# Performance work log

Measured on AMD Instinct MI355X. Metric: run time of the kernel, lower is better.

## Reference

```python
import jax, jax.numpy as jnp
import numpy as np

DIM = 2048
N_HEADS = 32
N_KV_HEADS = 8
HEAD_DIM = DIM // N_HEADS  # 64
N_REP = N_HEADS // N_KV_HEADS
ROPE_BASE = 10000.0


def rope_tables(seq_len, dim):
    inv_freq = 1.0 / (ROPE_BASE ** (jnp.arange(0, dim, 2, dtype=jnp.float32) / dim))
    t = jnp.arange(seq_len, dtype=jnp.float32)
    freqs = jnp.outer(t, inv_freq)            # [S, dim/2]
    emb = jnp.concatenate([freqs, freqs], -1)  # [S, dim]
    return jnp.cos(emb), jnp.sin(emb)          # each [S, dim]


def rotate_half(x):
    x1, x2 = jnp.split(x, 2, axis=-1)
    return jnp.concatenate([-x2, x1], axis=-1)


def setup_inputs() -> dict:
    key = jax.random.key(0)
    k_x, k_q, k_k, k_v, k_o = jax.random.split(key, 5)
    B, S = 2, 2048
    scale = 0.02
    x = jax.random.normal(k_x, (B, S, DIM), dtype=jnp.float32)
    # torch Linear weights are [out, in]
    w_q = jax.random.normal(k_q, (N_HEADS * HEAD_DIM, DIM), dtype=jnp.float32) * scale
    w_k = jax.random.normal(k_k, (N_KV_HEADS * HEAD_DIM, DIM), dtype=jnp.float32) * scale
    w_v = jax.random.normal(k_v, (N_KV_HEADS * HEAD_DIM, DIM), dtype=jnp.float32) * scale
    w_o = jax.random.normal(k_o, (DIM, N_HEADS * HEAD_DIM), dtype=jnp.float32) * scale
    return {"x": x, "w_q": w_q, "w_k": w_k, "w_v": w_v, "w_o": w_o}


def reference(x, w_q, w_k, w_v, w_o):
    B, S, _ = x.shape
    # projections (torch Linear: x @ W^T), reshape to [B, H, S, D]
    q = jnp.einsum('bsd,ed->bse', x, w_q).reshape(B, S, N_HEADS, HEAD_DIM).transpose(0, 2, 1, 3)
    k = jnp.einsum('bsd,ed->bse', x, w_k).reshape(B, S, N_KV_HEADS, HEAD_DIM).transpose(0, 2, 1, 3)
    v = jnp.einsum('bsd,ed->bse', x, w_v).reshape(B, S, N_KV_HEADS, HEAD_DIM).transpose(0, 2, 1, 3)
    # RoPE
    cos, sin = rope_tables(S, HEAD_DIM)  # [S, D]
    cos = cos[None, None]
    sin = sin[None, None]
    q = q * cos + rotate_half(q) * sin
    k = k * cos + rotate_half(k) * sin
    # GQA: expand kv heads (repeat_interleave along head dim)
    k = jnp.repeat(k, N_REP, axis=1)
    v = jnp.repeat(v, N_REP, axis=1)
    # attention
    scores = jnp.einsum('bhqd,bhkd->bhqk', q, k) / jnp.sqrt(jnp.float32(HEAD_DIM))
    attn = jax.nn.softmax(scores, axis=-1)
    out = jnp.einsum('bhqk,bhkd->bhqd', attn, v)
    out = out.transpose(0, 2, 1, 3).reshape(B, S, N_HEADS * HEAD_DIM)
    return jnp.einsum('bse,de->bsd', out, w_o)
```

## Files before the change

kernel.cpp:

```cpp
#include <hip/hip_runtime.h>
#include <hip/hip_bf16.h>

typedef __attribute__((ext_vector_type(8))) short bf16x8;
typedef __attribute__((ext_vector_type(4))) short bf16x4s;
typedef __attribute__((ext_vector_type(4))) float f32x4;
typedef __attribute__((ext_vector_type(2))) unsigned int u32x2;
typedef unsigned int u32;

#define DIM 2048
#define NH 32
#define NKV 8
#define HD 64
#define BB 2
#define SS 2048
#define MROWS (BB*SS)
#define NQKV 3072
#define KDIM 2048
#define L2E 1.44269504f

__device__ __forceinline__ short f2bf(float f){
  u32 u = __float_as_uint(f);
  u32 r = u + 0x7fffu + ((u >> 16) & 1u);
  return (short)(r >> 16);
}
__device__ __forceinline__ float bf2f(short s){
  return __uint_as_float(((u32)(unsigned short)s) << 16);
}

__device__ __forceinline__ void gload16(const void* g, void* l){
  __builtin_amdgcn_global_load_lds((const __attribute__((address_space(1))) u32*)g,
                                   (__attribute__((address_space(3))) u32*)l, 16, 0, 0);
}

__global__ __launch_bounds__(256) void cvt_all_kernel(const float* __restrict__ x,
                                                      const float* __restrict__ wq,
                                                      const float* __restrict__ wk,
                                                      const float* __restrict__ wv,
                                                      const float* __restrict__ wo,
                                                      short* __restrict__ xb,
                                                      short* __restrict__ wqkvb,
                                                      short* __restrict__ wob,
                                                      float* __restrict__ cosT,
                                                      float* __restrict__ sinT){
  int bid = blockIdx.x;
  if (bid >= 18432){
    int idx = (bid-18432)*256 + threadIdx.x;
    int s = idx >> 5, i = idx & 31;
    float inv = powf(10000.f, -(float)i * (1.f/32.f));
    float f = (float)s * inv;
    cosT[idx] = cosf(f);
    sinT[idx] = sinf(f);
    return;
  }
  int i = bid*256 + threadIdx.x;
  const float* src; short* dst; int off;
  if      (bid <  8192){ src = x;  dst = xb;              off = 0; }
  else if (bid < 12288){ src = wq; dst = wqkvb;           off = 2097152; }
  else if (bid < 13312){ src = wk; dst = wqkvb+2048*2048; off = 3145728; }
  else if (bid < 14336){ src = wv; dst = wqkvb+2560*2048; off = 3407872; }
  else                 { src = wo; dst = wob;             off = 3670016; }
  int j = i - off;
  f32x4 v = ((const f32x4*)src)[j];
  bf16x4s o;
  #pragma unroll
  for (int t=0;t<4;++t) o[t] = f2bf(v[t]);
  ((bf16x4s*)dst)[j] = o;
}

__global__ __launch_bounds__(256) void vT_kernel(const short* __restrict__ qkv,
                                                 short* __restrict__ Vtg){
  __shared__ short T[64*72];
  const int tid = threadIdx.x;
  const int s0 = blockIdx.x*64, hkv = blockIdx.y, b = blockIdx.z;
  const short* vbase = qkv + (size_t)b*SS*NQKV + DIM + NKV*HD + hkv*HD;
  #pragma unroll
  for (int cc=0; cc<2; ++cc){
    int c = tid + cc*256;
    int s = c >> 3, dc = c & 7;
    bf16x8 v = *(const bf16x8*)(vbase + (size_t)(s0+s)*NQKV + dc*8);
    #pragma unroll
    for (int i=0;i<8;++i) T[(dc*8+i)*72 + s] = v[i];
  }
  __syncthreads();
  short* obase = Vtg + ((size_t)(b*NKV + hkv)*64)*SS;
  #pragma unroll
  for (int cc=0; cc<2; ++cc){
    int c = tid + cc*256;
    int d = c >> 3, sc = c & 7;
    *(bf16x8*)(obase + (size_t)d*SS + s0 + sc*8) = *(const bf16x8*)&T[d*72 + sc*8];
  }
}

__global__ __launch_bounds__(256) void gemm_bt_kernel(const short* __restrict__ A,
                                                      const short* __restrict__ Bm,
                                                      short* __restrict__ C,
                                                      int ldc, int K,
                                                      const float* __restrict__ cosT,
                                                      const float* __restrict__ sinT,
                                                      int rope){
  __shared__ short As[128*64];
  __shared__ short Bs[128*64];
  const int tid = threadIdx.x;
  const int wave = tid >> 6, lane = tid & 63;
  const int g = lane >> 4, r16 = lane & 15;
  const int m0 = blockIdx.y * 128, n0 = blockIdx.x * 128;
  const int wr = wave >> 1, wc = wave & 1;
  f32x4 acc[4][4] = {};
  for (int k0 = 0; k0 < K; k0 += 64){
    #pragma unroll
    for (int it = 0; it < 4; ++it){
      int ch = it*256 + wave*64 + lane;
      int row = ch >> 3, kc = ch & 7;
      int skc = kc ^ (row & 7);
      gload16(A  + (size_t)(m0+row)*K + k0 + skc*8, (char*)As + it*4096 + wave*1024);
      gload16(Bm + (size_t)(n0+row)*K + k0 + skc*8, (char*)Bs + it*4096 + wave*1024);
    }
    __syncthreads();
    #pragma unroll
    for (int kk=0; kk<2; ++kk){
      bf16x8 a[4], b[4];
      #pragma unroll
      for (int i=0;i<4;++i){
        int Ra = wr*64 + i*16 + r16;
        a[i] = *(const bf16x8*)((const char*)As + Ra*128 + ((((kk<<2)+g) ^ (Ra&7)) << 4));
      }
      #pragma unroll
      for (int j=0;j<4;++j){
        int Rb = wc*64 + j*16 + r16;
        b[j] = *(const bf16x8*)((const char*)Bs + Rb*128 + ((((kk<<2)+g) ^ (Rb&7)) << 4));
      }
      #pragma unroll
      for (int i=0;i<4;++i)
        #pragma unroll
        for (int j=0;j<4;++j)
          acc[i][j] = __builtin_amdgcn_mfma_f32_16x16x32_bf16(a[i], b[j], acc[i][j], 0, 0, 0);
    }
    __syncthreads();
  }
  if (rope && n0 < 2560){
    float qsc = (n0 < 2048) ? 0.125f : 1.0f;
    #pragma unroll
    for (int i=0;i<4;++i)
      #pragma unroll
      for (int r=0;r<4;++r){
        int row = m0 + wr*64 + i*16 + g*4 + r;
        int s = row & (SS-1);
        #pragma unroll
        for (int j=0;j<2;++j){
          int col = n0 + wc*64 + j*16 + r16;
          float c  = cosT[(s<<5) + (col&31)];
          float sn = sinT[(s<<5) + (col&31)];
          float x1 = acc[i][j][r], x2 = acc[i][j+2][r];
          C[(size_t)row*ldc + col]      = f2bf((x1*c - x2*sn)*qsc);
          C[(size_t)row*ldc + col + 32] = f2bf((x2*c + x1*sn)*qsc);
        }
      }
  } else {
    #pragma unroll
    for (int i=0;i<4;++i)
      #pragma unroll
      for (int j=0;j<4;++j)
        #pragma unroll
        for (int r=0;r<4;++r){
          int row = m0 + wr*64 + i*16 + g*4 + r;
          int col = n0 + wc*64 + j*16 + r16;
          C[(size_t)row*ldc + col] = f2bf(acc[i][j][r]);
        }
  }
}

__global__ __launch_bounds__(256) void gemm_btf_kernel(const short* __restrict__ A,
                                                       const short* __restrict__ Bm,
                                                       float* __restrict__ C,
                                                       int ldc, int K){
  __shared__ short As[128*64];
  __shared__ short Bs[128*64];
  const int tid = threadIdx.x;
  const int wave = tid >> 6, lane = tid & 63;
  const int g = lane >> 4, r16 = lane & 15;
  const int m0 = blockIdx.y * 128, n0 = blockIdx.x * 128;
  const int wr = wave >> 1, wc = wave & 1;
  f32x4 acc[4][4] = {};
  for (int k0 = 0; k0 < K; k0 += 64){
    #pragma unroll
    for (int it = 0; it < 4; ++it){
      int ch = it*256 + wave*64 + lane;
      int row = ch >> 3, kc = ch & 7;
      int skc = kc ^ (row & 7);
      gload16(A  + (size_t)(m0+row)*K + k0 + skc*8, (char*)As + it*4096 + wave*1024);
      gload16(Bm + (size_t)(n0+row)*K + k0 + skc*8, (char*)Bs + it*4096 + wave*1024);
    }
    __syncthreads();
    #pragma unroll
    for (int kk=0; kk<2; ++kk){
      bf16x8 a[4], b[4];
      #pragma unroll
      for (int i=0;i<4;++i){
        int Ra = wr*64 + i*16 + r16;
        a[i] = *(const bf16x8*)((const char*)As + Ra*128 + ((((kk<<2)+g) ^ (Ra&7)) << 4));
      }
      #pragma unroll
      for (int j=0;j<4;++j){
        int Rb = wc*64 + j*16 + r16;
        b[j] = *(const bf16x8*)((const char*)Bs + Rb*128 + ((((kk<<2)+g) ^ (Rb&7)) << 4));
      }
      #pragma unroll
      for (int i=0;i<4;++i)
        #pragma unroll
        for (int j=0;j<4;++j)
          acc[i][j] = __builtin_amdgcn_mfma_f32_16x16x32_bf16(a[i], b[j], acc[i][j], 0, 0, 0);
    }
    __syncthreads();
  }
  #pragma unroll
  for (int i=0;i<4;++i)
    #pragma unroll
    for (int j=0;j<4;++j)
      #pragma unroll
      for (int r=0;r<4;++r){
        int row = m0 + wr*64 + i*16 + g*4 + r;
        int col = n0 + wc*64 + j*16 + r16;
        C[(size_t)row*ldc + col] = acc[i][j][r];
      }
}

__global__ __launch_bounds__(1024) void attn_kernel(const short* __restrict__ qkv,
                                                    const short* __restrict__ Vtg,
                                                    short* __restrict__ outb){
  __shared__ short Ks[64*64];
  __shared__ short Vt[64*64];
  __shared__ short Ps[16*16*72];
  const int tid = threadIdx.x;
  const int wave = tid >> 6, lane = tid & 63;
  const int g = lane >> 4, r16 = lane & 15;
  const int qt = blockIdx.x, h = blockIdx.y, b = blockIdx.z;
  const int hkv = h >> 2;
  const size_t row0 = (size_t)b * SS;
  const int qrow0 = qt*256 + wave*16;
  const short* qbase  = qkv + (row0 + qrow0)*NQKV + h*HD;
  const short* kbase  = qkv + row0*NQKV + DIM + hkv*HD;
  const short* vtbase = Vtg + ((size_t)(b*NKV + hkv)*64)*SS;

  bf16x8 qf[2];
  #pragma unroll
  for (int kk=0;kk<2;++kk)
    qf[kk] = *(const bf16x8*)(qbase + (size_t)r16*NQKV + kk*32 + g*8);

  f32x4 oaccT[4] = {};
  float M = -6.0e29f;
  float lrow = 0.f;

  short* pwv = &Ps[wave*16*72];

  const bool isK = (tid < 512);
  const int u = isK ? tid : (tid - 512);
  const int trow = u >> 3, tc3 = u & 7;
  const size_t goff = isK ? ((size_t)trow*NQKV + ((tc3 ^ (trow&7)) << 3))
                          : ((size_t)trow*SS   + ((tc3 ^ (trow&7)) << 3));
  const short* gsrc = isK ? kbase : vtbase;
  char* ldst = (isK ? (char*)Ks : (char*)Vt) + u*16;

  auto LOADR = [&](int s0, bf16x8& r){
    r = *(const bf16x8*)(gsrc + goff + (isK ? (size_t)s0*NQKV : (size_t)s0));
  };
  auto WRITE = [&](bf16x8 r){ *(bf16x8*)ldst = r; };

  { bf16x8 r0; LOADR(0, r0); WRITE(r0); }
  __syncthreads();

  const int NT = SS/64;
  for (int t = 0; t < NT; ++t){
    bool more = (t+1 < NT);
    bf16x8 rn;
    if (more) LOADR((t+1)*64, rn);

    f32x4 sacc[4];
    __builtin_amdgcn_s_setprio(1);
    #pragma unroll
    for (int t2=0;t2<4;++t2){
      f32x4 cacc = {};
      #pragma unroll
      for (int kk=0;kk<2;++kk){
        int krow = t2*16 + r16;
        const bf16x8* kp = (const bf16x8*)((const char*)Ks + krow*128 +
                            ((((kk<<2)+g) ^ (krow&7)) << 4));
        cacc = __builtin_amdgcn_mfma_f32_16x16x32_bf16(*kp, qf[kk], cacc, 0,0,0);
      }
      sacc[t2] = cacc;
    }
    __builtin_amdgcn_s_setprio(0);

    float m01 = fmaxf(fmaxf(sacc[0][0], sacc[0][1]), fmaxf(sacc[0][2], sacc[0][3]));
    float m23 = fmaxf(fmaxf(sacc[1][0], sacc[1][1]), fmaxf(sacc[1][2], sacc[1][3]));
    float m45 = fmaxf(fmaxf(sacc[2][0], sacc[2][1]), fmaxf(sacc[2][2], sacc[2][3]));
    float m67 = fmaxf(fmaxf(sacc[3][0], sacc[3][1]), fmaxf(sacc[3][2], sacc[3][3]));
    float mx = fmaxf(fmaxf(m01, m23), fmaxf(m45, m67));
    mx = fmaxf(mx, __shfl_xor(mx, 16));
    mx = fmaxf(mx, __shfl_xor(mx, 32));
    float mxl = mx * L2E;
    if (__any(mxl > M + 11.5f)){
      float Mnew = fmaxf(M, mxl);
      float al;
      { float a = M - Mnew; asm("v_exp_f32 %0, %1" : "=v"(al) : "v"(a)); }
      lrow *= al;
      #pragma unroll
      for (int j=0;j<4;++j)
        #pragma unroll
        for (int r=0;r<4;++r) oaccT[j][r] *= al;
      M = Mnew;
    }
    float s4[4] = {0.f,0.f,0.f,0.f};
    u32 pb[4][2];
    #pragma unroll
    for (int t2=0;t2<4;++t2){
      float p[4];
      #pragma unroll
      for (int r=0;r<4;++r){
        float a = fmaf(sacc[t2][r], L2E, -M);
        asm("v_exp_f32 %0, %1" : "=v"(p[r]) : "v"(a));
        s4[r] += p[r];
      }
      asm("v_cvt_pk_bf16_f32 %0, %1, %2" : "=v"(pb[t2][0]) : "v"(p[0]), "v"(p[1]));
      asm("v_cvt_pk_bf16_f32 %0, %1, %2" : "=v"(pb[t2][1]) : "v"(p[2]), "v"(p[3]));
    }
    float sum = (s4[0]+s4[1]) + (s4[2]+s4[3]);
    sum += __shfl_xor(sum, 16);
    sum += __shfl_xor(sum, 32);
    lrow += sum;

    #pragma unroll
    for (int t2=0;t2<4;++t2)
      *(u32x2*)&pwv[r16*72 + t2*16 + g*4] = (u32x2){pb[t2][0], pb[t2][1]};
    __builtin_amdgcn_s_setprio(1);
    #pragma unroll
    for (int kki=0;kki<2;++kki){
      bf16x8 pf = *(const bf16x8*)&pwv[r16*72 + 32*kki + g*8];
      #pragma unroll
      for (int j=0;j<4;++j){
        int d = j*16 + r16;
        const bf16x8* vp = (const bf16x8*)((const char*)Vt + d*128 +
                            ((((kki<<2)+g) ^ (d&7)) << 4));
        oaccT[j] = __builtin_amdgcn_mfma_f32_16x16x32_bf16(*vp, pf, oaccT[j], 0,0,0);
      }
    }
    __builtin_amdgcn_s_setprio(0);

    if (more){
      __syncthreads();
      WRITE(rn);
      __syncthreads();
    }
  }

  float inv = 1.0f / lrow;
  short* orow = outb + (row0 + qrow0 + r16)*(size_t)DIM + h*HD;
  #pragma unroll
  for (int j=0;j<4;++j){
    bf16x4s ov;
    #pragma unroll
    for (int r=0;r<4;++r) ov[r] = f2bf(oaccT[j][r]*inv);
    *(bf16x4s*)&orow[j*16 + g*4] = ov;
  }
}

extern "C" void kernel_launch(void* const* d_in, const int* in_sizes, int n_in,
                              void* d_out, int out_size, void* d_ws, size_t ws_size,
                              hipStream_t stream){
  const float* x  = (const float*)d_in[0];
  const float* wq = (const float*)d_in[1];
  const float* wk = (const float*)d_in[2];
  const float* wv = (const float*)d_in[3];
  const float* wo = (const float*)d_in[4];
  float* outf = (float*)d_out;

  char* ws = (char*)d_ws;
  short* wqkvb = (short*)(ws);
  short* attnb = (short*)(ws);
  short* wob   = (short*)(ws + 16777216);
  short* qkv   = (short*)(ws + 25165824);
  float* cosT  = (float*)(ws + 50331648);
  float* sinT  = (float*)(ws + 50593792);
  short* xb    = (short*)d_out;
  short* Vtg   = (short*)((char*)d_out + 16777216);

  cvt_all_kernel<<<18688, 256, 0, stream>>>(x, wq, wk, wv, wo, xb, wqkvb, wob, cosT, sinT);

  gemm_bt_kernel<<<dim3(NQKV/128, MROWS/128), 256, 0, stream>>>(xb, wqkvb, qkv, NQKV, KDIM,
                                                                cosT, sinT, 1);
  vT_kernel<<<dim3(SS/64, NKV, BB), 256, 0, stream>>>(qkv, Vtg);
  attn_kernel<<<dim3(SS/256, NH, BB), 1024, 0, stream>>>(qkv, Vtg, attnb);
  gemm_btf_kernel<<<dim3(DIM/128, MROWS/128), 256, 0, stream>>>(attnb, wob, outf, DIM, KDIM);
}
```

Baseline: 247.3 us.

## Process two 16-row query tiles per wave in attention kernel

Each wave now handles 32 query rows as two 16-row halves, so K fragments read from LDS are reused for two QK^T MFMAs. Blocks shrink from 1024 to 512 threads, and each thread loads both a K and a V chunk per tile. The aim is to reuse K/V LDS reads across more queries and cut per-block sync overhead. The cost is higher register pressure from doubled accumulators, and fewer waves are available to hide latency.

```diff
diff --git a/kernel.cpp b/kernel.cpp
--- a/kernel.cpp
+++ b/kernel.cpp
@@ -224,142 +224,167 @@
       }
 }
 
-__global__ __launch_bounds__(1024) void attn_kernel(const short* __restrict__ qkv,
-                                                    const short* __restrict__ Vtg,
-                                                    short* __restrict__ outb){
+__global__ __launch_bounds__(512) void attn_kernel(const short* __restrict__ qkv,
+                                                   const short* __restrict__ Vtg,
+                                                   short* __restrict__ outb){
   __shared__ short Ks[64*64];
   __shared__ short Vt[64*64];
-  __shared__ short Ps[16*16*72];
+  __shared__ short Ps[8*16*72];
   const int tid = threadIdx.x;
   const int wave = tid >> 6, lane = tid & 63;
   const int g = lane >> 4, r16 = lane & 15;
   const int qt = blockIdx.x, h = blockIdx.y, b = blockIdx.z;
   const int hkv = h >> 2;
   const size_t row0 = (size_t)b * SS;
-  const int qrow0 = qt*256 + wave*16;
+  const int qrow0 = qt*256 + wave*32;
   const short* qbase  = qkv + (row0 + qrow0)*NQKV + h*HD;
   const short* kbase  = qkv + row0*NQKV + DIM + hkv*HD;
   const short* vtbase = Vtg + ((size_t)(b*NKV + hkv)*64)*SS;
 
-  bf16x8 qf[2];
+  bf16x8 qfA[2], qfB[2];
   #pragma unroll
-  for (int kk=0;kk<2;++kk)
-    qf[kk] = *(const bf16x8*)(qbase + (size_t)r16*NQKV + kk*32 + g*8);
-
-  f32x4 oaccT[4] = {};
-  float M = -6.0e29f;
-  float lrow = 0.f;
+  for (int kk=0;kk<2;++kk){
+    qfA[kk] = *(const bf16x8*)(qbase + (size_t)r16*NQKV      + kk*32 + g*8);
+    qfB[kk] = *(const bf16x8*)(qbase + (size_t)(16+r16)*NQKV + kk*32 + g*8);
+  }
+
+  f32x4 oaccA[4] = {}, oaccB[4] = {};
+  float MA = -6.0e29f, MB = -6.0e29f;
+  float lA = 0.f, lB = 0.f;
 
   short* pwv = &Ps[wave*16*72];
 
-  const bool isK = (tid < 512);
-  const int u = isK ? tid : (tid - 512);
-  const int trow = u >> 3, tc3 = u & 7;
-  const size_t goff = isK ? ((size_t)trow*NQKV + ((tc3 ^ (trow&7)) << 3))
-                          : ((size_t)trow*SS   + ((tc3 ^ (trow&7)) << 3));
-  const short* gsrc = isK ? kbase : vtbase;
-  char* ldst = (isK ? (char*)Ks : (char*)Vt) + u*16;
-
-  auto LOADR = [&](int s0, bf16x8& r){
-    r = *(const bf16x8*)(gsrc + goff + (isK ? (size_t)s0*NQKV : (size_t)s0));
+  const int trow = tid >> 3, tc3 = tid & 7;
+  const size_t koff = (size_t)trow*NQKV + ((tc3 ^ (trow&7)) << 3);
+  const size_t voff = (size_t)trow*SS   + ((tc3 ^ (trow&7)) << 3);
+
+  auto LOADR = [&](int s0, bf16x8& kr, bf16x8& vr){
+    kr = *(const bf16x8*)(kbase + (size_t)s0*NQKV + koff);
+    vr = *(const bf16x8*)(vtbase + voff + s0);
   };
-  auto WRITE = [&](bf16x8 r){ *(bf16x8*)ldst = r; };
-
-  { bf16x8 r0; LOADR(0, r0); WRITE(r0); }
+  auto WRITE = [&](bf16x8 kr, bf16x8 vr){
+    *(bf16x8*)((char*)Ks + tid*16) = kr;
+    *(bf16x8*)((char*)Vt + tid*16) = vr;
+  };
+
+  { bf16x8 k0r, v0r; LOADR(0, k0r, v0r); WRITE(k0r, v0r); }
   __syncthreads();
 
   const int NT = SS/64;
   for (int t = 0; t < NT; ++t){
     bool more = (t+1 < NT);
-    bf16x8 rn;
-    if (more) LOADR((t+1)*64, rn);
-
-    f32x4 sacc[4];
+    bf16x8 krn, vrn;
+    if (more) LOADR((t+1)*64, krn, vrn);
+
+    f32x4 sA[4], sB[4];
     __builtin_amdgcn_s_setprio(1);
     #pragma unroll
     for (int t2=0;t2<4;++t2){
-      f32x4 cacc = {};
+      f32x4 ca = {}, cb = {};
       #pragma unroll
       for (int kk=0;kk<2;++kk){
         int krow = t2*16 + r16;
         const bf16x8* kp = (const bf16x8*)((const char*)Ks + krow*128 +
                             ((((kk<<2)+g) ^ (krow&7)) << 4));
-        cacc = __builtin_amdgcn_mfma_f32_16x16x32_bf16(*kp, qf[kk], cacc, 0,0,0);
-      }
-      sacc[t2] = cacc;
+        ca = __builtin_amdgcn_mfma_f32_16x16x32_bf16(*kp, qfA[kk], ca, 0,0,0);
+        cb = __builtin_amdgcn_mfma_f32_16x16x32_bf16(*kp, qfB[kk], cb, 0,0,0);
+      }
+      sA[t2] = ca; sB[t2] = cb;
     }
     __builtin_amdgcn_s_setprio(0);
 
-    float m01 = fmaxf(fmaxf(sacc[0][0], sacc[0][1]), fmaxf(sacc[0][2], sacc[0][3]));
-    float m23 = fmaxf(fmaxf(sacc[1][0], sacc[1][1]), fmaxf(sacc[1][2], sacc[1][3]));
-    float m45 = fmaxf(fmaxf(sacc[2][0], sacc[2][1]), fmaxf(sacc[2][2], sacc[2][3]));
-    float m67 = fmaxf(fmaxf(sacc[3][0], sacc[3][1]), fmaxf(sacc[3][2], sacc[3][3]));
-    float mx = fmaxf(fmaxf(m01, m23), fmaxf(m45, m67));
-    mx = fmaxf(mx, __shfl_xor(mx, 16));
-    mx = fmaxf(mx, __shfl_xor(mx, 32));
-    float mxl = mx * L2E;
-    if (__any(mxl > M + 11.5f)){
-      float Mnew = fmaxf(M, mxl);
-      float al;
-      { float a = M - Mnew; asm("v_exp_f32 %0, %1" : "=v"(al) : "v"(a)); }
-      lrow *= al;
-      #pragma unroll
-      for (int j=0;j<4;++j)
-        #pragma unroll
-        for (int r=0;r<4;++r) oaccT[j][r] *= al;
-      M = Mnew;
-    }
-    float s4[4] = {0.f,0.f,0.f,0.f};
-    u32 pb[4][2];
-    #pragma unroll
-    for (int t2=0;t2<4;++t2){
-      float p[4];
-      #pragma unroll
-      for (int r=0;r<4;++r){
-        float a = fmaf(sacc[t2][r], L2E, -M);
-        asm("v_exp_f32 %0, %1" : "=v"(p[r]) : "v"(a));
-        s4[r] += p[r];
-      }
-      asm("v_cvt_pk_bf16_f32 %0, %1, %2" : "=v"(pb[t2][0]) : "v"(p[0]), "v"(p[1]));
-      asm("v_cvt_pk_bf16_f32 %0, %1, %2" : "=v"(pb[t2][1]) : "v"(p[2]), "v"(p[3]));
-    }
-    float sum = (s4[0]+s4[1]) + (s4[2]+s4[3]);
-    sum += __shfl_xor(sum, 16);
-    sum += __shfl_xor(sum, 32);
-    lrow += sum;
-
-    #pragma unroll
-    for (int t2=0;t2<4;++t2)
-      *(u32x2*)&pwv[r16*72 + t2*16 + g*4] = (u32x2){pb[t2][0], pb[t2][1]};
-    __builtin_amdgcn_s_setprio(1);
-    #pragma unroll
-    for (int kki=0;kki<2;++kki){
-      bf16x8 pf = *(const bf16x8*)&pwv[r16*72 + 32*kki + g*8];
-      #pragma unroll
-      for (int j=0;j<4;++j){
-        int d = j*16 + r16;
-        const bf16x8* vp = (const bf16x8*)((const char*)Vt + d*128 +
-                            ((((kki<<2)+g) ^ (d&7)) << 4));
-        oaccT[j] = __builtin_amdgcn_mfma_f32_16x16x32_bf16(*vp, pf, oaccT[j], 0,0,0);
-      }
-    }
-    __builtin_amdgcn_s_setprio(0);
+    #pragma unroll
+    for (int half=0; half<2; ++half){
+      f32x4* sacc = half ? sB : sA;
+      f32x4* oaccT = half ? oaccB : oaccA;
+      float& M = half ? MB : MA;
+      float& lrow = half ? lB : lA;
+      const bf16x8* qq = half ? qfB : qfA;   (void)qq;
+
+      float m01 = fmaxf(fmaxf(sacc[0][0], sacc[0][1]), fmaxf(sacc[0][2], sacc[0][3]));
+      float m23 = fmaxf(fmaxf(sacc[1][0], sacc[1][1]), fmaxf(sacc[1][2], sacc[1][3]));
+      float m45 = fmaxf(fmaxf(sacc[2][0], sacc[2][1]), fmaxf(sacc[2][2], sacc[2][3]));
+      float m67 = fmaxf(fmaxf(sacc[3][0], sacc[3][1]), fmaxf(sacc[3][2], sacc[3][3]));
+      float mx = fmaxf(fmaxf(m01, m23), fmaxf(m45, m67));
+      mx = fmaxf(mx, __shfl_xor(mx, 16));
+      mx = fmaxf(mx, __shfl_xor(mx, 32));
+      float mxl = mx * L2E;
+      if (__any(mxl > M + 11.5f)){
+        float Mnew = fmaxf(M, mxl);
+        float al;
+        { float a = M - Mnew; asm("v_exp_f32 %0, %1" : "=v"(al) : "v"(a)); }
+        lrow *= al;
+        #pragma unroll
+        for (int j=0;j<4;++j)
+          #pragma unroll
+          for (int r=0;r<4;++r) oaccT[j][r] *= al;
+        M = Mnew;
+      }
+      float s4[4] = {0.f,0.f,0.f,0.f};
+      u32 pb[4][2];
+      #pragma unroll
+      for (int t2=0;t2<4;++t2){
+        float p[4];
+        #pragma unroll
+        for (int r=0;r<4;++r){
+          float a = fmaf(sacc[t2][r], L2E, -M);
+          asm("v_exp_f32 %0, %1" : "=v"(p[r]) : "v"(a));
+          s4[r] += p[r];
+        }
+        asm("v_cvt_pk_bf16_f32 %0, %1, %2" : "=v"(pb[t2][0]) : "v"(p[0]), "v"(p[1]));
+        asm("v_cvt_pk_bf16_f32 %0, %1, %2" : "=v"(pb[t2][1]) : "v"(p[2]), "v"(p[3]));
+      }
+      float sum = (s4[0]+s4[1]) + (s4[2]+s4[3]);
+      sum += __shfl_xor(sum, 16);
+      sum += __shfl_xor(sum, 32);
+      lrow += sum;
+
+      #pragma unroll
+      for (int t2=0;t2<4;++t2)
+        *(u32x2*)&pwv[r16*72 + t2*16 + g*4] = (u32x2){pb[t2][0], pb[t2][1]};
+      __builtin_amdgcn_s_setprio(1);
+      #pragma unroll
+      for (int kki=0;kki<2;++kki){
+        bf16x8 pf = *(const bf16x8*)&pwv[r16*72 + 32*kki + g*8];
+        #pragma unroll
+        for (int j=0;j<4;++j){
+          int d = j*16 + r16;
+          const bf16x8* vp = (const bf16x8*)((const char*)Vt + d*128 +
+                              ((((kki<<2)+g) ^ (d&7)) << 4));
+          oaccT[j] = __builtin_amdgcn_mfma_f32_16x16x32_bf16(*vp, pf, oaccT[j], 0,0,0);
+        }
+      }
+      __builtin_amdgcn_s_setprio(0);
+    }
 
     if (more){
       __syncthreads();
-      WRITE(rn);
+      WRITE(krn, vrn);
       __syncthreads();
     }
   }
 
-  float inv = 1.0f / lrow;
-  short* orow = outb + (row0 + qrow0 + r16)*(size_t)DIM + h*HD;
-  #pragma unroll
-  for (int j=0;j<4;++j){
-    bf16x4s ov;
-    #pragma unroll
-    for (int r=0;r<4;++r) ov[r] = f2bf(oaccT[j][r]*inv);
-    *(bf16x4s*)&orow[j*16 + g*4] = ov;
+  {
+    float inv = 1.0f / lA;
+    short* orow = outb + (row0 + qrow0 + r16)*(size_t)DIM + h*HD;
+    #pragma unroll
+    for (int j=0;j<4;++j){
+      bf16x4s ov;
+      #pragma unroll
+      for (int r=0;r<4;++r) ov[r] = f2bf(oaccA[j][r]*inv);
+      *(bf16x4s*)&orow[j*16 + g*4] = ov;
+    }
+  }
+  {
+    float inv = 1.0f / lB;
+    short* orow = outb + (row0 + qrow0 + 16 + r16)*(size_t)DIM + h*HD;
+    #pragma unroll
+    for (int j=0;j<4;++j){
+      bf16x4s ov;
+      #pragma unroll
+      for (int r=0;r<4;++r) ov[r] = f2bf(oaccB[j][r]*inv);
+      *(bf16x4s*)&orow[j*16 + g*4] = ov;
+    }
   }
 }
 
@@ -388,6 +413,6 @@
   gemm_bt_kernel<<<dim3(NQKV/128, MROWS/128), 256, 0, stream>>>(xb, wqkvb, qkv, NQKV, KDIM,
                                                                 cosT, sinT, 1);
   vT_kernel<<<dim3(SS/64, NKV, BB), 256, 0, stream>>>(qkv, Vtg);
-  attn_kernel<<<dim3(SS/256, NH, BB), 1024, 0, stream>>>(qkv, Vtg, attnb);
+  attn_kernel<<<dim3(SS/256, NH, BB), 512, 0, stream>>>(qkv, Vtg, attnb);
   gemm_btf_kernel<<<dim3(DIM/128, MROWS/128), 256, 0, stream>>>(attnb, wob, outf, DIM, KDIM);
 }
```

Measured after the change: 239.7 us. -3.0%, faster.
